# Optimization experiments

Hardware: AMD Instinct MI355X
Metric: run time of the kernel (lower is better)

## Reference

```python
import jax, jax.numpy as jnp
import numpy as np

N, E, F, S = 20000, 160000, 16, 8
ECC1, ECC2, ECC3 = 40, 24, 24
DS = [96, 256, 768, 512, 64, 1]


def setup_inputs() -> dict:
    key = jax.random.key(0)
    ks = iter(jax.random.split(key, 40))
    inp = {}
    inp["x"] = jax.random.normal(next(ks), (N, F), dtype=jnp.float32)
    inp["edge_index"] = jax.random.randint(next(ks), (E, 2), 0, N, dtype=jnp.int32)
    inp["e"] = jax.random.uniform(next(ks), (E, S), dtype=jnp.float32)

    def dense_p(k, fi, fo):
        return (jax.random.normal(k, (fi, fo), dtype=jnp.float32) * (1.0 / np.sqrt(fi)),
                jnp.zeros((fo,), dtype=jnp.float32))

    # ECCConv params: kernel_network dense (S -> F_in*F_out), root kernel, bias
    for i, (fi, fo) in enumerate([(F, ECC1), (ECC1, ECC2), (ECC2, ECC3)], start=1):
        We, be = dense_p(next(ks), S, fi * fo)
        root, _ = dense_p(next(ks), fi, fo)
        inp[f"We{i}"], inp[f"be{i}"] = We, be
        inp[f"root{i}"], inp[f"b{i}"] = root, jnp.zeros((fo,), dtype=jnp.float32)

    dims = [ECC3] + DS
    for i in range(6):
        W, b = dense_p(next(ks), dims[i], dims[i + 1])
        inp[f"Wd{i+1}"], inp[f"bd{i+1}"] = W, b
    return inp


def _ecc(h, src, tgt, e, We, be, root, b):
    fi, fo = root.shape
    # per-edge filter matrices from edge features: [E, F_in, F_out]
    K = (e @ We + be).reshape(e.shape[0], fi, fo)
    msg = jnp.einsum('ef,efo->eo', h[src], K)          # gather + per-edge matvec
    agg = jax.ops.segment_sum(msg, tgt, num_segments=h.shape[0])  # scatter-add
    return jax.nn.relu(agg + h @ root + b)


def reference(x, edge_index, e,
              We1, be1, root1, b1,
              We2, be2, root2, b2,
              We3, be3, root3, b3,
              Wd1, bd1, Wd2, bd2, Wd3, bd3, Wd4, bd4, Wd5, bd5, Wd6, bd6):
    src, tgt = edge_index[:, 0], edge_index[:, 1]
    h = _ecc(x, src, tgt, e, We1, be1, root1, b1)
    h = _ecc(h, src, tgt, e, We2, be2, root2, b2)
    h = _ecc(h, src, tgt, e, We3, be3, root3, b3)
    g = jnp.sum(h, axis=0, keepdims=True)  # GlobalSumPool (single mode) -> [1, 24]
    for W, b in [(Wd1, bd1), (Wd2, bd2), (Wd3, bd3), (Wd4, bd4), (Wd5, bd5)]:
        g = jax.nn.relu(g @ W + b)
    return g @ Wd6 + bd6  # [1, 1]
```

## Files before the change

### kernel.cpp

```cpp
#include <hip/hip_runtime.h>

constexpr int NN  = 20000;
constexpr int NE  = 160000;
constexpr int CAP = 32;
constexpr int TN2 = 8;
constexpr int NBM = 16;

__device__ inline void gstore(float* p, float v) {
    __hip_atomic_store(p, v, __ATOMIC_RELAXED, __HIP_MEMORY_SCOPE_AGENT);
}
__device__ inline float gload(const float* p) {
    return __hip_atomic_load(p, __ATOMIC_RELAXED, __HIP_MEMORY_SCOPE_AGENT);
}

__device__ inline void mbarrier(int* ctr, int target, bool wait) {
    __syncthreads();
    if (threadIdx.x == 0) {
        __threadfence();
        __hip_atomic_fetch_add(ctr, 1, __ATOMIC_ACQ_REL, __HIP_MEMORY_SCOPE_AGENT);
        if (wait)
            while (__hip_atomic_load(ctr, __ATOMIC_ACQUIRE, __HIP_MEMORY_SCOPE_AGENT) < target) {}
    }
    __syncthreads();
}

template<int FI, int FO2, int CH>
__device__ void stage_half(float* Wh, const float* __restrict__ We,
                           const float* __restrict__ be, const float* __restrict__ root,
                           int c0)
{
    constexpr int O4 = FO2 / 4;
    for (int t = threadIdx.x; t < FI * CH; t += 256) {
        const int f = t / CH, ccp = t % CH, cc = c0 + ccp;
        const int s = cc / O4, oq = cc % O4;
        const float4* src;
        if (s < 8)       src = (const float4*)(We + (size_t)s * FI * FO2 + f * FO2 + oq * 4);
        else if (s == 8) src = (const float4*)(be + f * FO2 + oq * 4);
        else             src = (const float4*)(root + f * FO2 + oq * 4);
        ((float4*)Wh)[t] = *src;
    }
}

template<int FI, int FO2, int CH>
__device__ void gemm_PL(const float* htile, const float* Wh,
                        const float* __restrict__ bias,
                        float* P_lds, float* __restrict__ seg9g, int n0, int c0)
{
    constexpr int O4 = FO2 / 4, PL = 9 * FO2;
    constexpr int TPN = 256 / TN2;
    constexpr int HS  = FI + 4;
    const int nl = threadIdx.x / TPN, lane = threadIdx.x % TPN;
    const float*  hr = &htile[nl * HS];
    const float4* W4 = (const float4*)Wh;
    for (int ccp = lane; ccp < CH; ccp += TPN) {
        const int cc = c0 + ccp;
        float4 a = {0.f, 0.f, 0.f, 0.f};
        #pragma unroll
        for (int f = 0; f < FI; f++) {
            const float  hf = hr[f];
            const float4 w  = W4[f * CH + ccp];
            a.x = fmaf(hf, w.x, a.x); a.y = fmaf(hf, w.y, a.y);
            a.z = fmaf(hf, w.z, a.z); a.w = fmaf(hf, w.w, a.w);
        }
        if (cc < 9 * O4) {
            *(float4*)&P_lds[nl * PL + cc * 4] = a;
        } else {
            const float4 b4 = ((const float4*)bias)[cc - 9 * O4];
            a.x += b4.x; a.y += b4.y; a.z += b4.z; a.w += b4.w;
            *(float4*)&seg9g[(size_t)(n0 + nl) * FO2 + (cc - 9 * O4) * 4] = a;
        }
    }
}

template<int FO2>
__device__ void push_phase(const float* P_lds, const int* offs_s,
                           const float* __restrict__ esort, float* __restrict__ msg,
                           float* scratch, int n0)
{
    constexpr int PL = 9 * FO2, OQ2 = FO2 / 4;
    float* elds = scratch;
    int*   esl  = (int*)(scratch + 2048);
    int*   enl  = esl + 256;
    const int tid = threadIdx.x;
    const int ET = offs_s[TN2];
    for (int T = tid; T < ET; T += 256) {
        int nl = 0;
        #pragma unroll
        for (int i = 1; i < TN2; i++) nl += (T >= offs_s[i]);
        const int j    = T - offs_s[nl];
        const int slot = (n0 + nl) * CAP + j;
        esl[T] = slot; enl[T] = nl;
        *(float4*)&elds[T * 8]     = *(const float4*)(esort + (size_t)slot * 8);
        *(float4*)&elds[T * 8 + 4] = *(const float4*)(esort + (size_t)slot * 8 + 4);
    }
    __syncthreads();
    for (int T = tid; T < ET * OQ2; T += 256) {
        const int ed = T / OQ2, oq = T % OQ2;
        const int nl = enl[ed], slot = esl[ed];
        const float* Pr = &P_lds[nl * PL + oq * 4];
        const float* ee = &elds[ed * 8];
        float4 m = *(const float4*)(Pr + 8 * FO2);
        #pragma unroll
        for (int s = 0; s < 8; s++) {
            const float  es = ee[s];
            const float4 w  = *(const float4*)(Pr + s * FO2);
            m.x = fmaf(es, w.x, m.x); m.y = fmaf(es, w.y, m.y);
            m.z = fmaf(es, w.z, m.z); m.w = fmaf(es, w.w, m.w);
        }
        *(float4*)&msg[(size_t)slot * FO2 + oq * 4] = m;
    }
}

__global__ __launch_bounds__(256)
void bucket_kernel(const int* __restrict__ eidx, const float* __restrict__ e,
                   int* __restrict__ cnt_s, int* __restrict__ cnt_t,
                   int* __restrict__ te_slot, float* __restrict__ esort)
{
    const int eid = blockIdx.x * 256 + threadIdx.x;
    const int2 st = ((const int2*)eidx)[eid];
    const int qs = atomicAdd(&cnt_s[st.x], 1);
    if (qs < CAP) {
        const int slot = st.x * CAP + qs;
        const float4* e4 = (const float4*)(e + (size_t)eid * 8);
        *(float4*)&esort[(size_t)slot * 8]     = e4[0];
        *(float4*)&esort[(size_t)slot * 8 + 4] = e4[1];
        const int qt = atomicAdd(&cnt_t[st.y], 1);
        if (qt < CAP) te_slot[st.y * CAP + qt] = slot;
    }
}

__global__ __launch_bounds__(256, 4)
void l1_push_kernel(const float* __restrict__ x,
                    const float* __restrict__ We1, const float* __restrict__ be1,
                    const float* __restrict__ root1, const float* __restrict__ b1,
                    const int* __restrict__ cnt_s, const float* __restrict__ esort,
                    float* __restrict__ seg9_1, float* __restrict__ msg1)
{
    constexpr int FI = 16, FO2 = 40, CH = 50;
    constexpr int WHF = FI * CH * 4;
    constexpr int PLF = TN2 * 9 * FO2;
    constexpr int HTF = TN2 * (FI + 4);
    __shared__ float smem[WHF + PLF + HTF];
    __shared__ int offs_s[TN2 + 1];
    float* Wh    = smem;
    float* P_lds = smem + WHF;
    float* htile = smem + WHF + PLF;
    const int tid = threadIdx.x;
    const int n0  = blockIdx.x * TN2;

    if (tid == 0) {
        int a = 0;
        for (int i = 0; i < TN2; i++) { offs_s[i] = a; a += min(cnt_s[n0 + i], CAP); }
        offs_s[TN2] = a;
    }
    stage_half<FI, FO2, CH>(Wh, We1, be1, root1, 0);
    for (int t = tid; t < TN2 * 4; t += 256) {
        const int nl = t / 4, fq = t % 4;
        *(float4*)&htile[nl * 20 + fq * 4] =
            *(const float4*)(x + (size_t)(n0 + nl) * 16 + fq * 4);
    }
    __syncthreads();
    gemm_PL<FI, FO2, CH>(htile, Wh, b1, P_lds, seg9_1, n0, 0);
    __syncthreads();
    stage_half<FI, FO2, CH>(Wh, We1, be1, root1, CH);
    __syncthreads();
    gemm_PL<FI, FO2, CH>(htile, Wh, b1, P_lds, seg9_1, n0, CH);
    __syncthreads();
    push_phase<FO2>(P_lds, offs_s, esort, msg1, Wh, n0);
}

template<int FI, int FO2, int CHP>
__global__ __launch_bounds__(256, 4)
void gather_gemm_push_kernel(const float* __restrict__ msg_prev,
                             const int* __restrict__ cnt_t, const int* __restrict__ te_slot,
                             const float* __restrict__ seg9_prev,
                             const float* __restrict__ We, const float* __restrict__ be,
                             const float* __restrict__ root, const float* __restrict__ bias,
                             const int* __restrict__ cnt_s, const float* __restrict__ esort,
                             float* __restrict__ seg9_next, float* __restrict__ msg_next)
{
    constexpr int C4    = 10 * FO2 / 4;
    constexpr int NPASS = C4 / CHP;
    constexpr int OQi   = FI / 4, HS = FI + 4;
    constexpr int WHF   = FI * CHP * 4;
    constexpr int PLF   = TN2 * 9 * FO2;
    constexpr int HTF   = TN2 * HS;
    __shared__ float smem[WHF + PLF + HTF];
    __shared__ int tslot[TN2 * CAP];
    __shared__ int offs_s[TN2 + 1];
    float* Wh    = smem;
    float* P_lds = smem + WHF;
    float* htile = smem + WHF + PLF;
    const int tid = threadIdx.x;
    const int n0  = blockIdx.x * TN2;

    if (tid == 0) {
        int a = 0;
        for (int i = 0; i < TN2; i++) { offs_s[i] = a; a += min(cnt_s[n0 + i], CAP); }
        offs_s[TN2] = a;
    }
    for (int t = tid; t < TN2 * CAP; t += 256) {
        const int nl = t / CAP, k = t % CAP;
        const int dd = min(cnt_t[n0 + nl], CAP);
        tslot[t] = (k < dd) ? te_slot[n0 * CAP + t] : -1;
    }
    stage_half<FI, FO2, CHP>(Wh, We, be, root, 0);
    for (int t = tid; t < TN2 * OQi; t += 256) {
        const int nl = t / OQi, oq = t % OQi;
        *(float4*)&htile[nl * HS + oq * 4] =
            *(const float4*)(seg9_prev + (size_t)(n0 + nl) * FI + oq * 4);
    }
    __syncthreads();

    for (int T = tid; T < TN2 * OQi; T += 256) {
        const int nl = T / OQi, oq = T % OQi;
        const int d = min(cnt_t[n0 + nl], CAP);
        float4 acc = *(float4*)&htile[nl * HS + oq * 4];
        const int* ts = &tslot[nl * CAP];
        for (int k0 = 0; k0 < CAP; k0 += 8) {
            if (k0 >= d) break;
            int sl[8]; float4 v[8];
            #pragma unroll
            for (int u = 0; u < 8; u++) {
                sl[u] = ts[k0 + u];
                const int sc = sl[u] < 0 ? 0 : sl[u];
                v[u] = *(const float4*)(msg_prev + (size_t)sc * FI + oq * 4);
            }
            #pragma unroll
            for (int u = 0; u < 8; u++) {
                if (sl[u] >= 0) {
                    acc.x += v[u].x; acc.y += v[u].y;
                    acc.z += v[u].z; acc.w += v[u].w;
                }
            }
        }
        acc.x = fmaxf(acc.x, 0.f); acc.y = fmaxf(acc.y, 0.f);
        acc.z = fmaxf(acc.z, 0.f); acc.w = fmaxf(acc.w, 0.f);
        *(float4*)&htile[nl * HS + oq * 4] = acc;
    }
    __syncthreads();

    #pragma unroll
    for (int p = 0; p < NPASS; p++) {
        if (p > 0) {
            __syncthreads();
            stage_half<FI, FO2, CHP>(Wh, We, be, root, p * CHP);
            __syncthreads();
        }
        gemm_PL<FI, FO2, CHP>(htile, Wh, bias, P_lds, seg9_next, n0, p * CHP);
    }
    __syncthreads();
    push_phase<FO2>(P_lds, offs_s, esort, msg_next, Wh, n0);
}

__global__ __launch_bounds__(256)
void msg_colsum_kernel(const float* __restrict__ msg, const int* __restrict__ cnt_t,
                       const int* __restrict__ te_slot, const float* __restrict__ seg9,
                       float* __restrict__ g)
{
    constexpr int FO = 24, OQ = 6;
    __shared__ int tslot[TN2 * CAP];
    __shared__ float gl[FO];
    const int tid = threadIdx.x;
    const int n0  = blockIdx.x * TN2;

    if (tid < FO) gl[tid] = 0.f;
    for (int t = tid; t < TN2 * CAP; t += 256) {
        const int nl = t / CAP, k = t % CAP;
        const int dd = min(cnt_t[n0 + nl], CAP);
        tslot[t] = (k < dd) ? te_slot[n0 * CAP + t] : -1;
    }
    __syncthreads();

    for (int T = tid; T < TN2 * OQ; T += 256) {
        const int nl = T / OQ, oq = T % OQ;
        const int d = min(cnt_t[n0 + nl], CAP);
        float4 acc = *(const float4*)(seg9 + (size_t)(n0 + nl) * FO + oq * 4);
        const int* ts = &tslot[nl * CAP];
        for (int k0 = 0; k0 < CAP; k0 += 8) {
            if (k0 >= d) break;
            int sl[8]; float4 v[8];
            #pragma unroll
            for (int u = 0; u < 8; u++) {
                sl[u] = ts[k0 + u];
                const int sc = sl[u] < 0 ? 0 : sl[u];
                v[u] = *(const float4*)(msg + (size_t)sc * FO + oq * 4);
            }
            #pragma unroll
            for (int u = 0; u < 8; u++) {
                if (sl[u] >= 0) {
                    acc.x += v[u].x; acc.y += v[u].y;
                    acc.z += v[u].z; acc.w += v[u].w;
                }
            }
        }
        atomicAdd(&gl[oq * 4 + 0], fmaxf(acc.x, 0.f));
        atomicAdd(&gl[oq * 4 + 1], fmaxf(acc.y, 0.f));
        atomicAdd(&gl[oq * 4 + 2], fmaxf(acc.z, 0.f));
        atomicAdd(&gl[oq * 4 + 3], fmaxf(acc.w, 0.f));
    }
    __syncthreads();
    if (tid < FO) unsafeAtomicAdd(&g[tid], gl[tid]);
}

__global__ __launch_bounds__(256)
void mlp_kernel(const float* __restrict__ g, int* __restrict__ ctr,
                const float* __restrict__ Wd1, const float* __restrict__ bd1,
                const float* __restrict__ Wd2, const float* __restrict__ bd2,
                const float* __restrict__ Wd3, const float* __restrict__ bd3,
                const float* __restrict__ Wd4, const float* __restrict__ bd4,
                const float* __restrict__ Wd5, const float* __restrict__ bd5,
                const float* __restrict__ Wd6, const float* __restrict__ bd6,
                float* __restrict__ m3, float* __restrict__ m4,
                float* __restrict__ out)
{
    __shared__ float v0[768];
    __shared__ float v1[96];
    __shared__ float red[256];
    const int tid = threadIdx.x, b = blockIdx.x;

    if (tid < 24) v0[tid] = g[tid];
    __syncthreads();
    if (tid < 96) {
        float a = bd1[tid];
        #pragma unroll
        for (int i = 0; i < 24; i++) a = fmaf(v0[i], Wd1[i * 96 + tid], a);
        v1[tid] = fmaxf(a, 0.f);
    }
    __syncthreads();
    {
        float a = bd2[tid];
        #pragma unroll
        for (int i = 0; i < 96; i++) a = fmaf(v1[i], Wd2[i * 256 + tid], a);
        red[tid] = fmaxf(a, 0.f);
    }
    __syncthreads();
    v0[tid] = red[tid];
    __syncthreads();

    if (tid < 192) {
        const int o = b * 48 + (tid % 48), kg = tid / 48;
        float a = 0.f;
        #pragma unroll 8
        for (int i = kg * 64; i < kg * 64 + 64; i++)
            a = fmaf(v0[i], Wd3[(size_t)i * 768 + o], a);
        red[tid] = a;
    }
    __syncthreads();
    if (tid < 48) {
        float s = bd3[b * 48 + tid] + red[tid] + red[48 + tid] + red[96 + tid] + red[144 + tid];
        gstore(&m3[b * 48 + tid], fmaxf(s, 0.f));
    }
    mbarrier(ctr, 1 * NBM, true);

    for (int i = tid; i < 768; i += 256) v0[i] = gload(&m3[i]);
    __syncthreads();
    {
        const int o = b * 32 + (tid & 31), kg = tid >> 5;
        float a = 0.f;
        #pragma unroll 8
        for (int i = kg * 96; i < kg * 96 + 96; i++)
            a = fmaf(v0[i], Wd4[(size_t)i * 512 + o], a);
        red[tid] = a;
    }
    __syncthreads();
    if (tid < 32) {
        float s = bd4[b * 32 + tid];
        #pragma unroll
        for (int k = 0; k < 8; k++) s += red[k * 32 + tid];
        gstore(&m4[b * 32 + tid], fmaxf(s, 0.f));
    }
    mbarrier(ctr, 2 * NBM, b == 0);

    if (b == 0) {
        for (int i = tid; i < 512; i += 256) v0[i] = gload(&m4[i]);
        __syncthreads();
        {
            const int o = tid & 63, kg = tid >> 6;
            float a = 0.f;
            #pragma unroll 8
            for (int i = kg * 128; i < kg * 128 + 128; i++)
                a = fmaf(v0[i], Wd5[(size_t)i * 64 + o], a);
            red[tid] = a;
        }
        __syncthreads();
        if (tid < 64) {
            float s = bd5[tid] + red[tid] + red[64 + tid] + red[128 + tid] + red[192 + tid];
            float v = fmaxf(s, 0.f) * Wd6[tid];
            #pragma unroll
            for (int off = 32; off > 0; off >>= 1)
                v += __shfl_down(v, off, 64);
            if (tid == 0) out[0] = v + bd6[0];
        }
    }
}

extern "C" void kernel_launch(void* const* d_in, const int* in_sizes, int n_in,
                              void* d_out, int out_size, void* d_ws, size_t ws_size,
                              hipStream_t stream)
{
    const float* x     = (const float*)d_in[0];
    const int*   eidx  = (const int*)  d_in[1];
    const float* e     = (const float*)d_in[2];
    const float* We1   = (const float*)d_in[3];  const float* be1 = (const float*)d_in[4];
    const float* root1 = (const float*)d_in[5];  const float* b1  = (const float*)d_in[6];
    const float* We2   = (const float*)d_in[7];  const float* be2 = (const float*)d_in[8];
    const float* root2 = (const float*)d_in[9];  const float* b2  = (const float*)d_in[10];
    const float* We3   = (const float*)d_in[11]; const float* be3 = (const float*)d_in[12];
    const float* root3 = (const float*)d_in[13]; const float* b3  = (const float*)d_in[14];
    const float* Wd1 = (const float*)d_in[15]; const float* bd1 = (const float*)d_in[16];
    const float* Wd2 = (const float*)d_in[17]; const float* bd2 = (const float*)d_in[18];
    const float* Wd3 = (const float*)d_in[19]; const float* bd3 = (const float*)d_in[20];
    const float* Wd4 = (const float*)d_in[21]; const float* bd4 = (const float*)d_in[22];
    const float* Wd5 = (const float*)d_in[23]; const float* bd5 = (const float*)d_in[24];
    const float* Wd6 = (const float*)d_in[25]; const float* bd6 = (const float*)d_in[26];

    int*   wi      = (int*)d_ws;
    float* wf      = (float*)d_ws;
    int*   cnt_s   = wi;
    int*   cnt_t   = wi + 20000;
    float* g       = wf + 40000;
    int*   mctr    = wi + 40064;
    float* m3      = wf + 40096;
    float* m4      = m3 + 768;
    int*   te_slot = wi + 41376;
    float* esort   = wf + 681376;
    float* seg9_1  = wf + 5801376;
    float* seg9_2  = wf + 6601376;
    float* seg9_3  = wf + 7081376;
    float* msg1    = wf + 7561376;
    float* msg3    = msg1;
    float* msg2    = wf + 33161376;

    hipMemsetAsync(d_ws, 0, (size_t)41376 * sizeof(float), stream);

    bucket_kernel<<<625, 256, 0, stream>>>(eidx, e, cnt_s, cnt_t, te_slot, esort);

    l1_push_kernel<<<NN / TN2, 256, 0, stream>>>(x, We1, be1, root1, b1,
                                                 cnt_s, esort, seg9_1, msg1);

    gather_gemm_push_kernel<40, 24, 30><<<NN / TN2, 256, 0, stream>>>(
        msg1, cnt_t, te_slot, seg9_1, We2, be2, root2, b2,
        cnt_s, esort, seg9_2, msg2);

    gather_gemm_push_kernel<24, 24, 60><<<NN / TN2, 256, 0, stream>>>(
        msg2, cnt_t, te_slot, seg9_2, We3, be3, root3, b3,
        cnt_s, esort, seg9_3, msg3);

    msg_colsum_kernel<<<NN / TN2, 256, 0, stream>>>(msg3, cnt_t, te_slot, seg9_3, g);

    mlp_kernel<<<NBM, 256, 0, stream>>>(g, mctr,
                                        Wd1, bd1, Wd2, bd2, Wd3, bd3,
                                        Wd4, bd4, Wd5, bd5, Wd6, bd6,
                                        m3, m4, (float*)d_out);
}
```

Before: 254.9 us.

## Prefetch edge features before GEMM and fuse colsum with MLP via grid barrier

Edge-feature staging into LDS now gets its own dedicated buffers and is issued before the per-node GEMM passes, so its global loads overlap with compute instead of running serially before the push phase. The gather kernel reads seg9_prev directly into the accumulator instead of staging it through htile. Layer 3 switches to a smaller weight chunk (30) so the larger LDS footprint still fits. The column-sum and MLP kernels are merged into one launch: an atomic counter barrier across all blocks means only the first 16 blocks continue into the MLP, which saves a launch but puts a spin-wait on the tail.

Result: slower. 310.8 us (+21.9%).

```diff
diff --git a/kernel.cpp b/kernel.cpp
--- a/kernel.cpp
+++ b/kernel.cpp
@@ -4,6 +4,7 @@
 constexpr int NE  = 160000;
 constexpr int CAP = 32;
 constexpr int TN2 = 8;
+constexpr int NT  = NN / TN2;
 constexpr int NBM = 16;
 
 __device__ inline void gstore(float* p, float v) {
@@ -72,18 +73,11 @@
     }
 }
 
-template<int FO2>
-__device__ void push_phase(const float* P_lds, const int* offs_s,
-                           const float* __restrict__ esort, float* __restrict__ msg,
-                           float* scratch, int n0)
-{
-    constexpr int PL = 9 * FO2, OQ2 = FO2 / 4;
-    float* elds = scratch;
-    int*   esl  = (int*)(scratch + 2048);
-    int*   enl  = esl + 256;
-    const int tid = threadIdx.x;
+__device__ void stage_elds(const int* offs_s, const float* __restrict__ esort,
+                           float* elds, int* esl, int* enl, int n0)
+{
     const int ET = offs_s[TN2];
-    for (int T = tid; T < ET; T += 256) {
+    for (int T = threadIdx.x; T < ET; T += 256) {
         int nl = 0;
         #pragma unroll
         for (int i = 1; i < TN2; i++) nl += (T >= offs_s[i]);
@@ -93,8 +87,16 @@
         *(float4*)&elds[T * 8]     = *(const float4*)(esort + (size_t)slot * 8);
         *(float4*)&elds[T * 8 + 4] = *(const float4*)(esort + (size_t)slot * 8 + 4);
     }
-    __syncthreads();
-    for (int T = tid; T < ET * OQ2; T += 256) {
+}
+
+template<int FO2>
+__device__ void push_compute(const float* P_lds, const int* offs_s,
+                             const float* elds, const int* esl, const int* enl,
+                             float* __restrict__ msg)
+{
+    constexpr int PL = 9 * FO2, OQ2 = FO2 / 4;
+    const int ET = offs_s[TN2];
+    for (int T = threadIdx.x; T < ET * OQ2; T += 256) {
         const int ed = T / OQ2, oq = T % OQ2;
         const int nl = enl[ed], slot = esl[ed];
         const float* Pr = &P_lds[nl * PL + oq * 4];
@@ -137,14 +139,12 @@
                     float* __restrict__ seg9_1, float* __restrict__ msg1)
 {
     constexpr int FI = 16, FO2 = 40, CH = 50;
-    constexpr int WHF = FI * CH * 4;
-    constexpr int PLF = TN2 * 9 * FO2;
-    constexpr int HTF = TN2 * (FI + 4);
-    __shared__ float smem[WHF + PLF + HTF];
-    __shared__ int offs_s[TN2 + 1];
-    float* Wh    = smem;
-    float* P_lds = smem + WHF;
-    float* htile = smem + WHF + PLF;
+    __shared__ float Wh[FI * CH * 4];
+    __shared__ float P_lds[TN2 * 9 * FO2];
+    __shared__ float htile[TN2 * (FI + 4)];
+    __shared__ float elds[2048];
+    __shared__ int   esl[256], enl[256];
+    __shared__ int   offs_s[TN2 + 1];
     const int tid = threadIdx.x;
     const int n0  = blockIdx.x * TN2;
 
@@ -160,13 +160,14 @@
             *(const float4*)(x + (size_t)(n0 + nl) * 16 + fq * 4);
     }
     __syncthreads();
+    stage_elds(offs_s, esort, elds, esl, enl, n0);
     gemm_PL<FI, FO2, CH>(htile, Wh, b1, P_lds, seg9_1, n0, 0);
     __syncthreads();
     stage_half<FI, FO2, CH>(Wh, We1, be1, root1, CH);
     __syncthreads();
     gemm_PL<FI, FO2, CH>(htile, Wh, b1, P_lds, seg9_1, n0, CH);
     __syncthreads();
-    push_phase<FO2>(P_lds, offs_s, esort, msg1, Wh, n0);
+    push_compute<FO2>(P_lds, offs_s, elds, esl, enl, msg1);
 }
 
 template<int FI, int FO2, int CHP>
@@ -182,15 +183,13 @@
     constexpr int C4    = 10 * FO2 / 4;
     constexpr int NPASS = C4 / CHP;
     constexpr int OQi   = FI / 4, HS = FI + 4;
-    constexpr int WHF   = FI * CHP * 4;
-    constexpr int PLF   = TN2 * 9 * FO2;
-    constexpr int HTF   = TN2 * HS;
-    __shared__ float smem[WHF + PLF + HTF];
-    __shared__ int tslot[TN2 * CAP];
-    __shared__ int offs_s[TN2 + 1];
-    float* Wh    = smem;
-    float* P_lds = smem + WHF;
-    float* htile = smem + WHF + PLF;
+    __shared__ float Wh[FI * CHP * 4];
+    __shared__ float P_lds[TN2 * 9 * FO2];
+    __shared__ float htile[TN2 * HS];
+    __shared__ float elds[2048];
+    __shared__ int   esl[256], enl[256];
+    __shared__ int   tslot[TN2 * CAP];
+    __shared__ int   offs_s[TN2 + 1];
     const int tid = threadIdx.x;
     const int n0  = blockIdx.x * TN2;
 
@@ -205,17 +204,13 @@
         tslot[t] = (k < dd) ? te_slot[n0 * CAP + t] : -1;
     }
     stage_half<FI, FO2, CHP>(Wh, We, be, root, 0);
-    for (int t = tid; t < TN2 * OQi; t += 256) {
-        const int nl = t / OQi, oq = t % OQi;
-        *(float4*)&htile[nl * HS + oq * 4] =
-            *(const float4*)(seg9_prev + (size_t)(n0 + nl) * FI + oq * 4);
-    }
-    __syncthreads();
-
+    __syncthreads();
+
+    stage_elds(offs_s, esort, elds, esl, enl, n0);
     for (int T = tid; T < TN2 * OQi; T += 256) {
         const int nl = T / OQi, oq = T % OQi;
         const int d = min(cnt_t[n0 + nl], CAP);
-        float4 acc = *(float4*)&htile[nl * HS + oq * 4];
+        float4 acc = *(const float4*)(seg9_prev + (size_t)(n0 + nl) * FI + oq * 4);
         const int* ts = &tslot[nl * CAP];
         for (int k0 = 0; k0 < CAP; k0 += 8) {
             if (k0 >= d) break;
@@ -240,29 +235,39 @@
     }
     __syncthreads();
 
+    gemm_PL<FI, FO2, CHP>(htile, Wh, bias, P_lds, seg9_next, n0, 0);
     #pragma unroll
-    for (int p = 0; p < NPASS; p++) {
-        if (p > 0) {
-            __syncthreads();
-            stage_half<FI, FO2, CHP>(Wh, We, be, root, p * CHP);
-            __syncthreads();
-        }
+    for (int p = 1; p < NPASS; p++) {
+        __syncthreads();
+        stage_half<FI, FO2, CHP>(Wh, We, be, root, p * CHP);
+        __syncthreads();
         gemm_PL<FI, FO2, CHP>(htile, Wh, bias, P_lds, seg9_next, n0, p * CHP);
     }
     __syncthreads();
-    push_phase<FO2>(P_lds, offs_s, esort, msg_next, Wh, n0);
+    push_compute<FO2>(P_lds, offs_s, elds, esl, enl, msg_next);
 }
 
 __global__ __launch_bounds__(256)
-void msg_colsum_kernel(const float* __restrict__ msg, const int* __restrict__ cnt_t,
+void colsum_mlp_kernel(const float* __restrict__ msg, const int* __restrict__ cnt_t,
                        const int* __restrict__ te_slot, const float* __restrict__ seg9,
-                       float* __restrict__ g)
+                       float* __restrict__ g, int* __restrict__ ctr,
+                       const float* __restrict__ Wd1, const float* __restrict__ bd1,
+                       const float* __restrict__ Wd2, const float* __restrict__ bd2,
+                       const float* __restrict__ Wd3, const float* __restrict__ bd3,
+                       const float* __restrict__ Wd4, const float* __restrict__ bd4,
+                       const float* __restrict__ Wd5, const float* __restrict__ bd5,
+                       const float* __restrict__ Wd6, const float* __restrict__ bd6,
+                       float* __restrict__ m3, float* __restrict__ m4,
+                       float* __restrict__ out)
 {
     constexpr int FO = 24, OQ = 6;
-    __shared__ int tslot[TN2 * CAP];
+    __shared__ int   tslot[TN2 * CAP];
     __shared__ float gl[FO];
-    const int tid = threadIdx.x;
-    const int n0  = blockIdx.x * TN2;
+    __shared__ float v0[768];
+    __shared__ float v1[96];
+    __shared__ float red[256];
+    const int tid = threadIdx.x, b = blockIdx.x;
+    const int n0  = b * TN2;
 
     if (tid < FO) gl[tid] = 0.f;
     for (int t = tid; t < TN2 * CAP; t += 256) {
@@ -271,7 +276,6 @@
         tslot[t] = (k < dd) ? te_slot[n0 * CAP + t] : -1;
     }
     __syncthreads();
-
     for (int T = tid; T < TN2 * OQ; T += 256) {
         const int nl = T / OQ, oq = T % OQ;
         const int d = min(cnt_t[n0 + nl], CAP);
@@ -301,25 +305,11 @@
     }
     __syncthreads();
     if (tid < FO) unsafeAtomicAdd(&g[tid], gl[tid]);
-}
-
-__global__ __launch_bounds__(256)
-void mlp_kernel(const float* __restrict__ g, int* __restrict__ ctr,
-                const float* __restrict__ Wd1, const float* __restrict__ bd1,
-                const float* __restrict__ Wd2, const float* __restrict__ bd2,
-                const float* __restrict__ Wd3, const float* __restrict__ bd3,
-                const float* __restrict__ Wd4, const float* __restrict__ bd4,
-                const float* __restrict__ Wd5, const float* __restrict__ bd5,
-                const float* __restrict__ Wd6, const float* __restrict__ bd6,
-                float* __restrict__ m3, float* __restrict__ m4,
-                float* __restrict__ out)
-{
-    __shared__ float v0[768];
-    __shared__ float v1[96];
-    __shared__ float red[256];
-    const int tid = threadIdx.x, b = blockIdx.x;
-
-    if (tid < 24) v0[tid] = g[tid];
+
+    mbarrier(ctr, NT, b < NBM);
+    if (b >= NBM) return;
+
+    if (tid < 24) v0[tid] = gload(&g[tid]);
     __syncthreads();
     if (tid < 96) {
         float a = bd1[tid];
@@ -351,7 +341,7 @@
         float s = bd3[b * 48 + tid] + red[tid] + red[48 + tid] + red[96 + tid] + red[144 + tid];
         gstore(&m3[b * 48 + tid], fmaxf(s, 0.f));
     }
-    mbarrier(ctr, 1 * NBM, true);
+    mbarrier(ctr, NT + 1 * NBM, true);
 
     for (int i = tid; i < 768; i += 256) v0[i] = gload(&m3[i]);
     __syncthreads();
@@ -370,7 +360,7 @@
         for (int k = 0; k < 8; k++) s += red[k * 32 + tid];
         gstore(&m4[b * 32 + tid], fmaxf(s, 0.f));
     }
-    mbarrier(ctr, 2 * NBM, b == 0);
+    mbarrier(ctr, NT + 2 * NBM, b == 0);
 
     if (b == 0) {
         for (int i = tid; i < 512; i += 256) v0[i] = gload(&m4[i]);
@@ -436,21 +426,20 @@
 
     bucket_kernel<<<625, 256, 0, stream>>>(eidx, e, cnt_s, cnt_t, te_slot, esort);
 
-    l1_push_kernel<<<NN / TN2, 256, 0, stream>>>(x, We1, be1, root1, b1,
-                                                 cnt_s, esort, seg9_1, msg1);
-
-    gather_gemm_push_kernel<40, 24, 30><<<NN / TN2, 256, 0, stream>>>(
+    l1_push_kernel<<<NT, 256, 0, stream>>>(x, We1, be1, root1, b1,
+                                           cnt_s, esort, seg9_1, msg1);
+
+    gather_gemm_push_kernel<40, 24, 30><<<NT, 256, 0, stream>>>(
         msg1, cnt_t, te_slot, seg9_1, We2, be2, root2, b2,
         cnt_s, esort, seg9_2, msg2);
 
-    gather_gemm_push_kernel<24, 24, 60><<<NN / TN2, 256, 0, stream>>>(
+    gather_gemm_push_kernel<24, 24, 30><<<NT, 256, 0, stream>>>(
         msg2, cnt_t, te_slot, seg9_2, We3, be3, root3, b3,
         cnt_s, esort, seg9_3, msg3);
 
-    msg_colsum_kernel<<<NN / TN2, 256, 0, stream>>>(msg3, cnt_t, te_slot, seg9_3, g);
-
-    mlp_kernel<<<NBM, 256, 0, stream>>>(g, mctr,
-                                        Wd1, bd1, Wd2, bd2, Wd3, bd3,
-                                        Wd4, bd4, Wd5, bd5, Wd6, bd6,
-                                        m3, m4, (float*)d_out);
-}
+    colsum_mlp_kernel<<<NT, 256, 0, stream>>>(msg3, cnt_t, te_slot, seg9_3,
+                                              g, mctr,
+                                              Wd1, bd1, Wd2, bd2, Wd3, bd3,
+                                              Wd4, bd4, Wd5, bd5, Wd6, bd6,
+                                              m3, m4, (float*)d_out);
+}
```
